# Kernel optimization log

Measured on AMD Instinct MI355X. Metric: run time of the kernel, lower is better.

## Reference

```python
import jax, jax.numpy as jnp
import numpy as np

B, T, D_IN, H = 128, 1024, 512, 1024  # batch, seq_len, input features, neurons


def setup_inputs() -> dict:
    key = jax.random.key(0)
    ks = jax.random.split(key, 10)
    glorot = lambda k, shape: jax.random.normal(k, shape, dtype=jnp.float32) * jnp.sqrt(2.0 / (shape[0] + shape[1]))
    return {
        "x": jax.random.normal(ks[0], (B, T, D_IN), dtype=jnp.float32),
        "W_z": glorot(ks[1], (D_IN, H)),
        "W_r": glorot(ks[2], (D_IN, H)),
        "W_h": glorot(ks[3], (D_IN, H)),
        "R_z": glorot(ks[4], (H, H)),
        "R_r": glorot(ks[5], (H, H)),
        "R_h": glorot(ks[6], (H, H)),
        "B_z": jax.random.uniform(ks[7], (H,), dtype=jnp.float32),
        "B_r": jax.random.uniform(ks[8], (H,), dtype=jnp.float32),
        "B_h": jax.random.uniform(ks[9], (H,), dtype=jnp.float32),
    }


def reference(x, W_z, W_r, W_h, R_z, R_r, R_h, B_z, B_r, B_h):
    # Time-major: [T, B, D_IN]
    xs = jnp.transpose(x, (1, 0, 2))

    def step(state, xt):
        z = jax.nn.sigmoid(xt @ W_z + state @ R_z + B_z)
        r = jax.nn.sigmoid(xt @ W_r + state @ R_r + B_r)
        h = jnp.tanh(xt @ W_h + (r * state) @ R_h + B_h)
        y = (1.0 - z) * state + z * h
        return y, None

    init = jnp.zeros((x.shape[0], W_z.shape[1]), dtype=x.dtype)
    final, _ = jax.lax.scan(step, init, xs)
    return final  # [B, H] (return_sequences=False)
```

## Files before the change

### kernel.cpp

```cpp
#include <hip/hip_runtime.h>
#include <hip/hip_bf16.h>


#define BB   128
#define TT   1024
#define DIN  512
#define HD   1024

typedef short short8 __attribute__((ext_vector_type(8)));
typedef float f32x4 __attribute__((ext_vector_type(4)));
typedef unsigned long long ull;

#define FLAGS_OFF 0
#define WT_OFF    16384
#define RT_OFF    (WT_OFF + 3*HD*DIN*2)
#define HBF_OFF   (RT_OFF + 3*HD*HD*2)
#define RH_OFF    (HBF_OFF + BB*HD*2)
#define XBF_OFF   (RH_OFF + BB*HD*2)
#define XBF_BYTES ((size_t)BB*TT*DIN*2)

__device__ __forceinline__ unsigned short f2bf(float f) {
    unsigned u = __builtin_bit_cast(unsigned, f);
    u = (u + 0x7FFFu + ((u >> 16) & 1u)) >> 16;
    return (unsigned short)u;
}

__device__ __forceinline__ ull pack4(const float* p) {
    return (ull)f2bf(p[0]) | ((ull)f2bf(p[1]) << 16) |
           ((ull)f2bf(p[2]) << 32) | ((ull)f2bf(p[3]) << 48);
}

__device__ __forceinline__ ull pack4v(float4 v) {
    return (ull)f2bf(v.x) | ((ull)f2bf(v.y) << 16) |
           ((ull)f2bf(v.z) << 32) | ((ull)f2bf(v.w) << 48);
}

__device__ __forceinline__ short8 ld8(const unsigned short* p) {
    return *(const short8*)p;
}

__device__ __forceinline__ ull ald(const ull* p) {
    return __hip_atomic_load(p, __ATOMIC_RELAXED, __HIP_MEMORY_SCOPE_AGENT);
}
__device__ __forceinline__ void ast(ull* p, ull v) {
    __hip_atomic_store(p, v, __ATOMIC_RELAXED, __HIP_MEMORY_SCOPE_AGENT);
}

#define MFMA(A, B, C) __builtin_amdgcn_mfma_f32_16x16x32_bf16((A), (B), (C), 0, 0, 0)

__global__ void pack_weights(const float* __restrict__ w0, const float* __restrict__ w1,
                             const float* __restrict__ w2, const float* __restrict__ r0,
                             const float* __restrict__ r1, const float* __restrict__ r2,
                             unsigned short* __restrict__ wt, unsigned short* __restrict__ rt) {
    int z = blockIdx.z;
    int K = (z < 3) ? DIN : HD;
    int kb = blockIdx.x * 32;
    if (kb >= K) return;
    int nb = blockIdx.y * 32;
    const float* src = (z == 0) ? w0 : (z == 1) ? w1 : (z == 2) ? w2
                     : (z == 3) ? r0 : (z == 4) ? r1 : r2;
    unsigned short* dst = (z < 3) ? (wt + (size_t)z * HD * DIN)
                                  : (rt + (size_t)(z - 3) * HD * HD);
    __shared__ float tile[32][33];
    int tx = threadIdx.x & 31, ty = threadIdx.x >> 5;
    for (int i = ty; i < 32; i += 8)
        tile[i][tx] = src[(size_t)(kb + i) * HD + nb + tx];
    __syncthreads();
    for (int i = ty; i < 32; i += 8)
        dst[(size_t)(nb + i) * K + kb + tx] = f2bf(tile[tx][i]);
}

__global__ void pack_x(const float* __restrict__ x, unsigned short* __restrict__ xbf,
                       long long n4) {
    long long i = (long long)blockIdx.x * blockDim.x + threadIdx.x;
    long long stride = (long long)gridDim.x * blockDim.x;
    const float4* xv = (const float4*)x;
    ull* o = (ull*)xbf;
    for (; i < n4; i += stride) o[i] = pack4v(xv[i]);
}

__launch_bounds__(512, 2)
__global__ void gru_persistent(const float* __restrict__ x,
                               const unsigned short* __restrict__ xbf,
                               const float* __restrict__ Bz, const float* __restrict__ Br,
                               const float* __restrict__ Bh,
                               const unsigned short* __restrict__ WT,
                               const unsigned short* __restrict__ RT,
                               unsigned short* __restrict__ hbf,
                               unsigned short* __restrict__ rhbf,
                               unsigned* __restrict__ flags,
                               float* __restrict__ out) {
    const int g = blockIdx.x;
    const int group  = g & 7;
    const int member = g >> 3;
    const int rowbase = group * 16;
    const int colbase = member * 32;
    const int tid  = threadIdx.x;
    const int w    = tid >> 6;
    const int lane = tid & 63;
    const int frow = lane & 15;
    const int fquad = lane >> 4;
    const int k0 = fquad * 8;

    const int gA = (w >> 2) & 1;
    const int cA = (w >> 1) & 1;
    const int hA = w & 1;
    const int cB = w & 1;
    const int xh = (w >> 1) & 1;

    __shared__ unsigned short xsh[16][520];
    __shared__ unsigned short hsh[16][1032];
    __shared__ float zbuf[16][36];
    __shared__ float rtmp[16][36];
    __shared__ float hstate[16][36];
    __shared__ float redA[2][2][4][64];
    __shared__ float redB[2][10][4][64];

    unsigned* gflags = flags + group * 32;

    if (tid < 128) {
        int row = tid >> 3, c4 = tid & 7;
        *(float4*)&hstate[row][c4 * 4] = make_float4(0.f, 0.f, 0.f, 0.f);
    }

    short8 wAx[8], wAh[16], wB0[4], wB1[4], wBx[8];
    {
        const unsigned short* wcolA = WT + ((size_t)gA * HD + colbase + cA * 16 + frow) * DIN;
        const unsigned short* rcolA = RT + ((size_t)gA * HD + colbase + cA * 16 + frow) * HD;
        #pragma unroll
        for (int i = 0; i < 8; ++i)  wAx[i] = ld8(wcolA + (hA * 8 + i) * 32 + k0);
        #pragma unroll
        for (int i = 0; i < 16; ++i) wAh[i] = ld8(rcolA + (hA * 16 + i) * 32 + k0);

        const unsigned short* rcolB0 = RT + ((size_t)2 * HD + colbase + frow) * HD;
        const unsigned short* rcolB1 = RT + ((size_t)2 * HD + colbase + 16 + frow) * HD;
        #pragma unroll
        for (int i = 0; i < 4; ++i) wB0[i] = ld8(rcolB0 + (w * 4 + i) * 32 + k0);
        #pragma unroll
        for (int i = 0; i < 4; ++i) wB1[i] = ld8(rcolB1 + (w * 4 + i) * 32 + k0);

        if (w < 4) {
            const unsigned short* wcolB = WT + ((size_t)2 * HD + colbase + cB * 16 + frow) * DIN;
            #pragma unroll
            for (int i = 0; i < 8; ++i) wBx[i] = ld8(wcolB + (xh * 8 + i) * 32 + k0);
        }
    }
    const float bvA = (gA == 0 ? Bz : Br)[colbase + cA * 16 + frow];
    const float bvB = Bh[colbase + (w & 1) * 16 + frow];

    const ull* hbf_u = (const ull*)hbf;
    const ull* rh_u  = (const ull*)rhbf;

#define STAGE_X(tt) do {                                                              \
        if (xbf) {                                                                    \
            const ull* xr = (const ull*)xbf;                                          \
            for (int i = tid; i < 2048; i += 512) {                                   \
                int row = i >> 7, c4 = i & 127;                                       \
                *(ull*)&xsh[row][c4 * 4] =                                            \
                    xr[((size_t)(rowbase + row) * TT + (tt)) * (DIN / 4) + c4];       \
            }                                                                         \
        } else {                                                                      \
            for (int i = tid; i < 2048; i += 512) {                                   \
                int row = i >> 7, c4 = i & 127;                                       \
                *(ull*)&xsh[row][c4 * 4] = pack4v(                                    \
                    ((const float4*)(x + ((size_t)(rowbase + row) * TT + (tt)) * DIN))[c4]); \
            }                                                                         \
        }                                                                             \
    } while (0)

    f32x4 xa0, xa1;
#define COMPUTE_XA() do {                                                             \
        f32x4 t0 = {0.f,0.f,0.f,0.f}, t1 = {0.f,0.f,0.f,0.f};                         \
        _Pragma("unroll")                                                             \
        for (int i = 0; i < 8; i += 2) {                                              \
            t0 = MFMA(ld8(&xsh[frow][(hA * 8 + i) * 32 + k0]), wAx[i], t0);           \
            t1 = MFMA(ld8(&xsh[frow][(hA * 8 + i + 1) * 32 + k0]), wAx[i + 1], t1);   \
        }                                                                             \
        xa0 = t0; xa1 = t1;                                                           \
    } while (0)

    STAGE_X(0);
    __syncthreads();
    COMPUTE_XA();

    unsigned phase = 0;

    for (int t = 0; t < TT; ++t) {
        ull hreg[8];
        {
            const int c8 = tid & 255;
            const int r0r = tid >> 8;
            #pragma unroll
            for (int j = 0; j < 8; ++j)
                hreg[j] = ald(hbf_u + (size_t)(rowbase + r0r + 2 * j) * 256 + c8);
        }
        if (w < 4) {
            f32x4 b0 = {0.f,0.f,0.f,0.f}, b1 = {0.f,0.f,0.f,0.f};
            #pragma unroll
            for (int i = 0; i < 8; i += 2) {
                b0 = MFMA(ld8(&xsh[frow][(xh * 8 + i) * 32 + k0]), wBx[i], b0);
                b1 = MFMA(ld8(&xsh[frow][(xh * 8 + i + 1) * 32 + k0]), wBx[i + 1], b1);
            }
            #pragma unroll
            for (int r4 = 0; r4 < 4; ++r4) redB[cB][8 + xh][r4][lane] = b0[r4] + b1[r4];
        }
        {
            const int c8 = tid & 255;
            const int r0r = tid >> 8;
            #pragma unroll
            for (int j = 0; j < 8; ++j)
                *(ull*)&hsh[r0r + 2 * j][c8 * 4] = hreg[j];
        }
        __syncthreads();

        {
            f32x4 a0 = xa0, a1 = xa1;
            #pragma unroll
            for (int i = 0; i < 16; i += 2) {
                a0 = MFMA(ld8(&hsh[frow][(hA * 16 + i) * 32 + k0]), wAh[i], a0);
                a1 = MFMA(ld8(&hsh[frow][(hA * 16 + i + 1) * 32 + k0]), wAh[i + 1], a1);
            }
            if (hA == 1) {
                #pragma unroll
                for (int r4 = 0; r4 < 4; ++r4)
                    redA[gA][cA][r4][lane] = a0[r4] + a1[r4];
            }
            __syncthreads();
            if (hA == 0) {
                const int c = cA * 16 + frow;
                #pragma unroll
                for (int r4 = 0; r4 < 4; ++r4) {
                    int row = fquad * 4 + r4;
                    float pre = a0[r4] + a1[r4] + redA[gA][cA][r4][lane] + bvA;
                    float sg = 1.f / (1.f + __expf(-pre));
                    if (gA == 0) zbuf[row][c] = sg;
                    else         rtmp[row][c] = sg * hstate[row][c];
                }
            }
        }
        __syncthreads();
        if (tid < 128) {
            int row = tid >> 3, c4 = tid & 7;
            ast((ull*)rhbf + (size_t)(rowbase + row) * 256 + (colbase >> 2) + c4,
                pack4(&rtmp[row][c4 * 4]));
        }
        __syncthreads();
        ++phase;
        if (tid == 0)
            __hip_atomic_store(gflags + member, phase,
                               __ATOMIC_RELAXED, __HIP_MEMORY_SCOPE_AGENT);
        if (t + 1 < TT) {
            STAGE_X(t + 1);
        }
        if (tid < 32) {
            while (__hip_atomic_load(gflags + tid, __ATOMIC_RELAXED,
                                     __HIP_MEMORY_SCOPE_AGENT) < phase)
                __builtin_amdgcn_s_sleep(1);
        }
        __syncthreads();

        {
            f32x4 b0 = {0.f,0.f,0.f,0.f}, b1 = {0.f,0.f,0.f,0.f};
            const ull* rrow = rh_u + (size_t)(rowbase + frow) * 256 + w * 32 + fquad * 2;
            union { ull u[2]; short8 s; } fr[4];
            #pragma unroll
            for (int i = 0; i < 4; ++i) {
                fr[i].u[0] = ald(rrow + i * 8);
                fr[i].u[1] = ald(rrow + i * 8 + 1);
            }
            #pragma unroll
            for (int i = 0; i < 4; ++i) {
                b0 = MFMA(fr[i].s, wB0[i], b0);
                b1 = MFMA(fr[i].s, wB1[i], b1);
            }
            #pragma unroll
            for (int r4 = 0; r4 < 4; ++r4) {
                redB[0][w][r4][lane] = b0[r4];
                redB[1][w][r4][lane] = b1[r4];
            }
            __syncthreads();
            if (w < 2) {
                const int c = w * 16 + frow;
                #pragma unroll
                for (int r4 = 0; r4 < 4; ++r4) {
                    int row = fquad * 4 + r4;
                    float pre = bvB;
                    #pragma unroll
                    for (int s = 0; s < 10; ++s) pre += redB[w][s][r4][lane];
                    float e = __expf(2.f * pre);
                    float ht = 1.f - 2.f / (e + 1.f);
                    float zv = zbuf[row][c];
                    float ho = hstate[row][c];
                    hstate[row][c] = ho + zv * (ht - ho);
                }
            }
        }
        __syncthreads();

        if (t + 1 < TT) {
            if (tid < 128) {
                int row = tid >> 3, c4 = tid & 7;
                ast((ull*)hbf + (size_t)(rowbase + row) * 256 + (colbase >> 2) + c4,
                    pack4(&hstate[row][c4 * 4]));
            }
            __syncthreads();
            ++phase;
            if (tid == 0)
                __hip_atomic_store(gflags + member, phase,
                                   __ATOMIC_RELAXED, __HIP_MEMORY_SCOPE_AGENT);
            COMPUTE_XA();
            if (tid < 32) {
                while (__hip_atomic_load(gflags + tid, __ATOMIC_RELAXED,
                                         __HIP_MEMORY_SCOPE_AGENT) < phase)
                    __builtin_amdgcn_s_sleep(1);
            }
            __syncthreads();
        }
    }

    if (tid < 128) {
        int row = tid >> 3, c4 = tid & 7;
        *(float4*)(out + (size_t)(rowbase + row) * HD + colbase + c4 * 4) =
            *(float4*)&hstate[row][c4 * 4];
    }
}

extern "C" void kernel_launch(void* const* d_in, const int* in_sizes, int n_in,
                              void* d_out, int out_size, void* d_ws, size_t ws_size,
                              hipStream_t stream) {
    const float* x  = (const float*)d_in[0];
    const float* Wz = (const float*)d_in[1];
    const float* Wr = (const float*)d_in[2];
    const float* Wh = (const float*)d_in[3];
    const float* Rz = (const float*)d_in[4];
    const float* Rr = (const float*)d_in[5];
    const float* Rh = (const float*)d_in[6];
    const float* Bz = (const float*)d_in[7];
    const float* Br = (const float*)d_in[8];
    const float* Bh = (const float*)d_in[9];

    char* ws = (char*)d_ws;
    unsigned*       flags = (unsigned*)(ws + FLAGS_OFF);
    unsigned short* WT    = (unsigned short*)(ws + WT_OFF);
    unsigned short* RT    = (unsigned short*)(ws + RT_OFF);
    unsigned short* hbf   = (unsigned short*)(ws + HBF_OFF);
    unsigned short* rhbf  = (unsigned short*)(ws + RH_OFF);

    const bool use_xbf = ws_size >= (size_t)XBF_OFF + XBF_BYTES;
    unsigned short* XBF = use_xbf ? (unsigned short*)(ws + XBF_OFF) : nullptr;

    hipMemsetAsync(ws + FLAGS_OFF, 0, 1024, stream);
    hipMemsetAsync(ws + HBF_OFF, 0, BB * HD * 2, stream);

    dim3 pgrid(HD / 32, HD / 32, 6);
    pack_weights<<<pgrid, 256, 0, stream>>>(Wz, Wr, Wh, Rz, Rr, Rh, WT, RT);
    if (use_xbf)
        pack_x<<<2048, 256, 0, stream>>>(x, XBF,
                                         (long long)((size_t)BB * TT * DIN / 4));

    gru_persistent<<<256, 512, 0, stream>>>(x, XBF, Bz, Br, Bh, WT, RT, hbf, rhbf,
                                            flags, (float*)d_out);
}
```

Before: 8.215 ms.

## Replace group-wide barriers with per-producer flag waits at point of use

Each thread (or wave) now waits only on the flags of the blocks whose hbf/rhbf slices it actually reads, right before loading them. This removes the all-32-flag spin plus __syncthreads after each publish, so a block can proceed once its specific producers are ready rather than after the whole group. It relies on relaxed atomics and a compiler barrier for ordering, and many threads now spin on flags concurrently, which adds polling traffic and some memory-ordering risk.

```diff
diff --git a/kernel.cpp b/kernel.cpp
--- a/kernel.cpp
+++ b/kernel.cpp
@@ -44,6 +44,9 @@
 }
 __device__ __forceinline__ void ast(ull* p, ull v) {
     __hip_atomic_store(p, v, __ATOMIC_RELAXED, __HIP_MEMORY_SCOPE_AGENT);
+}
+__device__ __forceinline__ unsigned aldf(const unsigned* p) {
+    return __hip_atomic_load(p, __ATOMIC_RELAXED, __HIP_MEMORY_SCOPE_AGENT);
 }
 
 #define MFMA(A, B, C) __builtin_amdgcn_mfma_f32_16x16x32_bf16((A), (B), (C), 0, 0, 0)
@@ -183,17 +186,20 @@
     __syncthreads();
     COMPUTE_XA();
 
-    unsigned phase = 0;
+    const int c8  = tid & 255;
+    const int r0r = tid >> 8;
+    const unsigned* myflag1 = gflags + (c8 >> 3);
 
     for (int t = 0; t < TT; ++t) {
+        if (t) {
+            const unsigned need = 2u * (unsigned)t;
+            while (aldf(myflag1) < need) __builtin_amdgcn_s_sleep(1);
+            asm volatile("" ::: "memory");
+        }
         ull hreg[8];
-        {
-            const int c8 = tid & 255;
-            const int r0r = tid >> 8;
-            #pragma unroll
-            for (int j = 0; j < 8; ++j)
-                hreg[j] = ald(hbf_u + (size_t)(rowbase + r0r + 2 * j) * 256 + c8);
-        }
+        #pragma unroll
+        for (int j = 0; j < 8; ++j)
+            hreg[j] = ald(hbf_u + (size_t)(rowbase + r0r + 2 * j) * 256 + c8);
         if (w < 4) {
             f32x4 b0 = {0.f,0.f,0.f,0.f}, b1 = {0.f,0.f,0.f,0.f};
             #pragma unroll
@@ -204,13 +210,9 @@
             #pragma unroll
             for (int r4 = 0; r4 < 4; ++r4) redB[cB][8 + xh][r4][lane] = b0[r4] + b1[r4];
         }
-        {
-            const int c8 = tid & 255;
-            const int r0r = tid >> 8;
-            #pragma unroll
-            for (int j = 0; j < 8; ++j)
-                *(ull*)&hsh[r0r + 2 * j][c8 * 4] = hreg[j];
-        }
+        #pragma unroll
+        for (int j = 0; j < 8; ++j)
+            *(ull*)&hsh[r0r + 2 * j][c8 * 4] = hreg[j];
         __syncthreads();
 
         {
@@ -239,27 +241,28 @@
             }
         }
         __syncthreads();
+
         if (tid < 128) {
             int row = tid >> 3, c4 = tid & 7;
             ast((ull*)rhbf + (size_t)(rowbase + row) * 256 + (colbase >> 2) + c4,
                 pack4(&rtmp[row][c4 * 4]));
         }
         __syncthreads();
-        ++phase;
         if (tid == 0)
-            __hip_atomic_store(gflags + member, phase,
+            __hip_atomic_store(gflags + member, 2u * (unsigned)t + 1u,
                                __ATOMIC_RELAXED, __HIP_MEMORY_SCOPE_AGENT);
         if (t + 1 < TT) {
             STAGE_X(t + 1);
         }
-        if (tid < 32) {
-            while (__hip_atomic_load(gflags + tid, __ATOMIC_RELAXED,
-                                     __HIP_MEMORY_SCOPE_AGENT) < phase)
-                __builtin_amdgcn_s_sleep(1);
-        }
-        __syncthreads();
 
         {
+            if (lane < 4) {
+                const unsigned need = 2u * (unsigned)t + 1u;
+                const unsigned* fp = gflags + 4 * w + lane;
+                while (aldf(fp) < need) __builtin_amdgcn_s_sleep(1);
+            }
+            asm volatile("" ::: "memory");
+
             f32x4 b0 = {0.f,0.f,0.f,0.f}, b1 = {0.f,0.f,0.f,0.f};
             const ull* rrow = rh_u + (size_t)(rowbase + frow) * 256 + w * 32 + fquad * 2;
             union { ull u[2]; short8 s; } fr[4];
@@ -304,17 +307,10 @@
                     pack4(&hstate[row][c4 * 4]));
             }
             __syncthreads();
-            ++phase;
             if (tid == 0)
-                __hip_atomic_store(gflags + member, phase,
+                __hip_atomic_store(gflags + member, 2u * (unsigned)t + 2u,
                                    __ATOMIC_RELAXED, __HIP_MEMORY_SCOPE_AGENT);
             COMPUTE_XA();
-            if (tid < 32) {
-                while (__hip_atomic_load(gflags + tid, __ATOMIC_RELAXED,
-                                         __HIP_MEMORY_SCOPE_AGENT) < phase)
-                    __builtin_amdgcn_s_sleep(1);
-            }
-            __syncthreads();
         }
     }
 
```

Measured after the change: 8.019 ms. 2.4% less time.

## Replace flag barriers with step-tagged data words for inter-block sync

Applied to the files above, without the earlier changes.

Each bf16 pair exchanged between blocks is packed with a timestep tag into a 64-bit word, in double-buffered hx/rx arrays. Consumers spin on the data itself until every tag matches, which removes the separate flag stores, flag polling and the extra __syncthreads around them. This shortens the critical path of each recurrent step. The cost is doubled exchange traffic (32 bits of payload per 64-bit word) and every thread polling many words, with retries under contention.

```diff
diff --git a/kernel.cpp b/kernel.cpp
--- a/kernel.cpp
+++ b/kernel.cpp
@@ -11,23 +11,17 @@
 typedef float f32x4 __attribute__((ext_vector_type(4)));
 typedef unsigned long long ull;
 
-#define FLAGS_OFF 0
 #define WT_OFF    16384
 #define RT_OFF    (WT_OFF + 3*HD*DIN*2)
-#define HBF_OFF   (RT_OFF + 3*HD*HD*2)
-#define RH_OFF    (HBF_OFF + BB*HD*2)
-#define XBF_OFF   (RH_OFF + BB*HD*2)
+#define HX_OFF    (RT_OFF + 3*HD*HD*2)
+#define RX_OFF    (HX_OFF + 2*BB*512*8)
+#define XBF_OFF   (RX_OFF + 2*BB*512*8)
 #define XBF_BYTES ((size_t)BB*TT*DIN*2)
 
 __device__ __forceinline__ unsigned short f2bf(float f) {
     unsigned u = __builtin_bit_cast(unsigned, f);
     u = (u + 0x7FFFu + ((u >> 16) & 1u)) >> 16;
     return (unsigned short)u;
-}
-
-__device__ __forceinline__ ull pack4(const float* p) {
-    return (ull)f2bf(p[0]) | ((ull)f2bf(p[1]) << 16) |
-           ((ull)f2bf(p[2]) << 32) | ((ull)f2bf(p[3]) << 48);
 }
 
 __device__ __forceinline__ ull pack4v(float4 v) {
@@ -86,9 +80,8 @@
                                const float* __restrict__ Bh,
                                const unsigned short* __restrict__ WT,
                                const unsigned short* __restrict__ RT,
-                               unsigned short* __restrict__ hbf,
-                               unsigned short* __restrict__ rhbf,
-                               unsigned* __restrict__ flags,
+                               ull* __restrict__ hx,
+                               ull* __restrict__ rx,
                                float* __restrict__ out) {
     const int g = blockIdx.x;
     const int group  = g & 7;
@@ -116,8 +109,6 @@
     __shared__ float redA[2][2][4][64];
     __shared__ float redB[2][10][4][64];
 
-    unsigned* gflags = flags + group * 32;
-
     if (tid < 128) {
         int row = tid >> 3, c4 = tid & 7;
         *(float4*)&hstate[row][c4 * 4] = make_float4(0.f, 0.f, 0.f, 0.f);
@@ -147,9 +138,6 @@
     }
     const float bvA = (gA == 0 ? Bz : Br)[colbase + cA * 16 + frow];
     const float bvB = Bh[colbase + (w & 1) * 16 + frow];
-
-    const ull* hbf_u = (const ull*)hbf;
-    const ull* rh_u  = (const ull*)rhbf;
 
 #define STAGE_X(tt) do {                                                              \
         if (xbf) {                                                                    \
@@ -183,17 +171,7 @@
     __syncthreads();
     COMPUTE_XA();
 
-    unsigned phase = 0;
-
     for (int t = 0; t < TT; ++t) {
-        ull hreg[8];
-        {
-            const int c8 = tid & 255;
-            const int r0r = tid >> 8;
-            #pragma unroll
-            for (int j = 0; j < 8; ++j)
-                hreg[j] = ald(hbf_u + (size_t)(rowbase + r0r + 2 * j) * 256 + c8);
-        }
         if (w < 4) {
             f32x4 b0 = {0.f,0.f,0.f,0.f}, b1 = {0.f,0.f,0.f,0.f};
             #pragma unroll
@@ -205,11 +183,21 @@
             for (int r4 = 0; r4 < 4; ++r4) redB[cB][8 + xh][r4][lane] = b0[r4] + b1[r4];
         }
         {
-            const int c8 = tid & 255;
-            const int r0r = tid >> 8;
-            #pragma unroll
-            for (int j = 0; j < 8; ++j)
-                *(ull*)&hsh[r0r + 2 * j][c8 * 4] = hreg[j];
+            const unsigned need = (unsigned)t;
+            const ull* hsrc = hx + ((size_t)(t & 1) * BB + rowbase) * 512 + tid;
+            ull v[16];
+            for (;;) {
+                bool ok = true;
+                #pragma unroll
+                for (int j = 0; j < 16; ++j) v[j] = ald(hsrc + j * 512);
+                #pragma unroll
+                for (int j = 0; j < 16; ++j) ok &= ((unsigned)(v[j] >> 32) == need);
+                if (ok) break;
+                __builtin_amdgcn_s_sleep(1);
+            }
+            #pragma unroll
+            for (int j = 0; j < 16; ++j)
+                *(unsigned*)&hsh[j][2 * tid] = (unsigned)v[j];
         }
         __syncthreads();
 
@@ -239,39 +227,49 @@
             }
         }
         __syncthreads();
-        if (tid < 128) {
-            int row = tid >> 3, c4 = tid & 7;
-            ast((ull*)rhbf + (size_t)(rowbase + row) * 256 + (colbase >> 2) + c4,
-                pack4(&rtmp[row][c4 * 4]));
-        }
-        __syncthreads();
-        ++phase;
-        if (tid == 0)
-            __hip_atomic_store(gflags + member, phase,
-                               __ATOMIC_RELAXED, __HIP_MEMORY_SCOPE_AGENT);
+
+        {
+            const ull tg = (ull)((unsigned)t + 1u) << 32;
+            if (tid < 128) {
+                int row = tid >> 3, q = tid & 7;
+                ull* dst = rx + ((size_t)(t & 1) * BB + rowbase + row) * 512
+                              + (colbase >> 1) + q * 2;
+                const float* rp = &rtmp[row][q * 4];
+                ast(dst,     (ull)f2bf(rp[0]) | ((ull)f2bf(rp[1]) << 16) | tg);
+                ast(dst + 1, (ull)f2bf(rp[2]) | ((ull)f2bf(rp[3]) << 16) | tg);
+            }
+        }
         if (t + 1 < TT) {
             STAGE_X(t + 1);
         }
-        if (tid < 32) {
-            while (__hip_atomic_load(gflags + tid, __ATOMIC_RELAXED,
-                                     __HIP_MEMORY_SCOPE_AGENT) < phase)
+
+        {
+            const unsigned need = (unsigned)t + 1u;
+            const ull* rsrc = rx + ((size_t)(t & 1) * BB + rowbase + frow) * 512
+                                 + 64 * w + 4 * fquad;
+            ull fr[4][4];
+            for (;;) {
+                bool ok = true;
+                #pragma unroll
+                for (int i = 0; i < 4; ++i)
+                    #pragma unroll
+                    for (int q = 0; q < 4; ++q) fr[i][q] = ald(rsrc + 16 * i + q);
+                #pragma unroll
+                for (int i = 0; i < 4; ++i)
+                    #pragma unroll
+                    for (int q = 0; q < 4; ++q)
+                        ok &= ((unsigned)(fr[i][q] >> 32) == need);
+                if (ok) break;
                 __builtin_amdgcn_s_sleep(1);
-        }
-        __syncthreads();
-
-        {
+            }
             f32x4 b0 = {0.f,0.f,0.f,0.f}, b1 = {0.f,0.f,0.f,0.f};
-            const ull* rrow = rh_u + (size_t)(rowbase + frow) * 256 + w * 32 + fquad * 2;
-            union { ull u[2]; short8 s; } fr[4];
             #pragma unroll
             for (int i = 0; i < 4; ++i) {
-                fr[i].u[0] = ald(rrow + i * 8);
-                fr[i].u[1] = ald(rrow + i * 8 + 1);
-            }
-            #pragma unroll
-            for (int i = 0; i < 4; ++i) {
-                b0 = MFMA(fr[i].s, wB0[i], b0);
-                b1 = MFMA(fr[i].s, wB1[i], b1);
+                union { unsigned u[4]; short8 s; } mk;
+                #pragma unroll
+                for (int q = 0; q < 4; ++q) mk.u[q] = (unsigned)fr[i][q];
+                b0 = MFMA(mk.s, wB0[i], b0);
+                b1 = MFMA(mk.s, wB1[i], b1);
             }
             #pragma unroll
             for (int r4 = 0; r4 < 4; ++r4) {
@@ -298,23 +296,16 @@
         __syncthreads();
 
         if (t + 1 < TT) {
+            const ull tg = (ull)((unsigned)t + 1u) << 32;
             if (tid < 128) {
-                int row = tid >> 3, c4 = tid & 7;
-                ast((ull*)hbf + (size_t)(rowbase + row) * 256 + (colbase >> 2) + c4,
-                    pack4(&hstate[row][c4 * 4]));
-            }
-            __syncthreads();
-            ++phase;
-            if (tid == 0)
-                __hip_atomic_store(gflags + member, phase,
-                                   __ATOMIC_RELAXED, __HIP_MEMORY_SCOPE_AGENT);
+                int row = tid >> 3, q = tid & 7;
+                ull* dst = hx + ((size_t)((t + 1) & 1) * BB + rowbase + row) * 512
+                              + (colbase >> 1) + q * 2;
+                const float* hp = &hstate[row][q * 4];
+                ast(dst,     (ull)f2bf(hp[0]) | ((ull)f2bf(hp[1]) << 16) | tg);
+                ast(dst + 1, (ull)f2bf(hp[2]) | ((ull)f2bf(hp[3]) << 16) | tg);
+            }
             COMPUTE_XA();
-            if (tid < 32) {
-                while (__hip_atomic_load(gflags + tid, __ATOMIC_RELAXED,
-                                         __HIP_MEMORY_SCOPE_AGENT) < phase)
-                    __builtin_amdgcn_s_sleep(1);
-            }
-            __syncthreads();
         }
     }
 
@@ -340,17 +331,15 @@
     const float* Bh = (const float*)d_in[9];
 
     char* ws = (char*)d_ws;
-    unsigned*       flags = (unsigned*)(ws + FLAGS_OFF);
-    unsigned short* WT    = (unsigned short*)(ws + WT_OFF);
-    unsigned short* RT    = (unsigned short*)(ws + RT_OFF);
-    unsigned short* hbf   = (unsigned short*)(ws + HBF_OFF);
-    unsigned short* rhbf  = (unsigned short*)(ws + RH_OFF);
+    unsigned short* WT = (unsigned short*)(ws + WT_OFF);
+    unsigned short* RT = (unsigned short*)(ws + RT_OFF);
+    ull*            HX = (ull*)(ws + HX_OFF);
+    ull*            RX = (ull*)(ws + RX_OFF);
 
     const bool use_xbf = ws_size >= (size_t)XBF_OFF + XBF_BYTES;
     unsigned short* XBF = use_xbf ? (unsigned short*)(ws + XBF_OFF) : nullptr;
 
-    hipMemsetAsync(ws + FLAGS_OFF, 0, 1024, stream);
-    hipMemsetAsync(ws + HBF_OFF, 0, BB * HD * 2, stream);
+    hipMemsetAsync(ws + HX_OFF, 0, (size_t)4 * BB * 512 * 8, stream);
 
     dim3 pgrid(HD / 32, HD / 32, 6);
     pack_weights<<<pgrid, 256, 0, stream>>>(Wz, Wr, Wh, Rz, Rr, Rh, WT, RT);
@@ -358,6 +347,6 @@
         pack_x<<<2048, 256, 0, stream>>>(x, XBF,
                                          (long long)((size_t)BB * TT * DIN / 4));
 
-    gru_persistent<<<256, 512, 0, stream>>>(x, XBF, Bz, Br, Bh, WT, RT, hbf, rhbf,
-                                            flags, (float*)d_out);
-}
+    gru_persistent<<<256, 512, 0, stream>>>(x, XBF, Bz, Br, Bh, WT, RT,
+                                            HX, RX, (float*)d_out);
+}
```

Measured after the change: 11.48 ms. +39.8%, slower.
